# Kernel tuning notes

Hardware: AMD Instinct MI355X
Metric: run time of the kernel (lower is better)

Reference implementation:

```python
import jax, jax.numpy as jnp
import numpy as np

N_NODES = 50000
N_EDGES = 800000
IN_DIM = 5
HID = (32, 64, 128, 64, 32)
OUT_DIM = 2
EPS = 1e-5  # nn.BatchNorm1d default eps


def _bn(x, g, b):
    # BatchNorm1d in training mode: batch (biased) statistics over nodes
    m = jnp.mean(x, axis=0)
    v = jnp.var(x, axis=0)
    return (x - m) * jax.lax.rsqrt(v + EPS) * g + b


def setup_inputs() -> dict:
    key = jax.random.key(0)
    ks = jax.random.split(key, 40)
    it = iter(range(40))
    def nrm(shape, s=0.1):
        return jax.random.normal(ks[next(it)], shape, jnp.float32) * s
    inp = {}
    inp["x"] = jax.random.normal(ks[next(it)], (N_NODES, IN_DIM), jnp.float32)
    inp["edge_index"] = jax.random.randint(ks[next(it)], (2, N_EDGES), 0, N_NODES, jnp.int32)
    # input embedding: Linear(5,32) -> ReLU -> BatchNorm1d(32)
    inp["emb_W"] = nrm((IN_DIM, HID[0]))
    inp["emb_b"] = jnp.zeros((HID[0],), jnp.float32)
    inp["emb_g"] = jnp.ones((HID[0],), jnp.float32)
    inp["emb_beta"] = jnp.zeros((HID[0],), jnp.float32)
    # 4 GraphConv blocks
    for i in range(len(HID) - 1):
        din, dout = HID[i], HID[i + 1]
        inp[f"b{i}_Wrel"] = nrm((din, dout))   # lin_rel weight (has bias)
        inp[f"b{i}_brel"] = jnp.zeros((dout,), jnp.float32)
        inp[f"b{i}_Wroot"] = nrm((din, dout))  # lin_root weight (no bias)
        inp[f"b{i}_g"] = jnp.ones((dout,), jnp.float32)
        inp[f"b{i}_beta"] = jnp.zeros((dout,), jnp.float32)
    # output MLP: Linear(32,16) -> ReLU -> Linear(16,2)
    inp["out_W1"] = nrm((HID[-1], HID[-1] // 2))
    inp["out_b1"] = jnp.zeros((HID[-1] // 2,), jnp.float32)
    inp["out_W2"] = nrm((HID[-1] // 2, OUT_DIM))
    inp["out_b2"] = jnp.zeros((OUT_DIM,), jnp.float32)
    return inp


def reference(x, edge_index,
              emb_W, emb_b, emb_g, emb_beta,
              b0_Wrel, b0_brel, b0_Wroot, b0_g, b0_beta,
              b1_Wrel, b1_brel, b1_Wroot, b1_g, b1_beta,
              b2_Wrel, b2_brel, b2_Wroot, b2_g, b2_beta,
              b3_Wrel, b3_brel, b3_Wroot, b3_g, b3_beta,
              out_W1, out_b1, out_W2, out_b2):
    src, dst = edge_index[0], edge_index[1]
    # input embedding: Linear -> ReLU -> BN
    h = jnp.maximum(x @ emb_W + emb_b, 0.0)
    h = _bn(h, emb_g, emb_beta)
    blocks = [
        (b0_Wrel, b0_brel, b0_Wroot, b0_g, b0_beta),
        (b1_Wrel, b1_brel, b1_Wroot, b1_g, b1_beta),
        (b2_Wrel, b2_brel, b2_Wroot, b2_g, b2_beta),
        (b3_Wrel, b3_brel, b3_Wroot, b3_g, b3_beta),
    ]
    for Wrel, brel, Wroot, g, beta in blocks:
        # GraphConv (aggr='add'): lin_rel(sum_{j in N(i)} x_j) + lin_root(x_i)
        agg = jax.ops.segment_sum(h[src], dst, num_segments=N_NODES)
        h = agg @ Wrel + brel + h @ Wroot
        # BN then ReLU (GNNBlock order)
        h = jnp.maximum(_bn(h, g, beta), 0.0)
    # output MLP
    h = jnp.maximum(h @ out_W1 + out_b1, 0.0)
    return h @ out_W2 + out_b2
```

## Files before the change

kernel.cpp:

```cpp
#include <hip/hip_runtime.h>

#define N_NODES 50000
#define N_EDGES 800000
#define BN_EPS 1e-5f

__device__ __forceinline__ void fma4(float4& a, float s, const float4& w) {
    a.x += s * w.x; a.y += s * w.y; a.z += s * w.z; a.w += s * w.w;
}
__device__ __forceinline__ void add4(float4& a, const float4& b) {
    a.x += b.x; a.y += b.y; a.z += b.z; a.w += b.w;
}

__global__ void zero_i(int* __restrict__ p, int n) {
    int i = blockIdx.x * blockDim.x + threadIdx.x;
    int stride = gridDim.x * blockDim.x;
    for (; i < n; i += stride) p[i] = 0;
}

__global__ void hist_kernel(const int* __restrict__ dst, int* __restrict__ cnt) {
    int i = blockIdx.x * blockDim.x + threadIdx.x;
    int stride = gridDim.x * blockDim.x;
    for (; i < N_EDGES; i += stride) atomicAdd(&cnt[dst[i]], 1);
}
__global__ void scan1_kernel(const int* __restrict__ cnt, int* __restrict__ rp,
                             int* __restrict__ bsum) {
    __shared__ int s[256];
    int t = threadIdx.x;
    int idx = blockIdx.x * 256 + t;
    int v = (idx < N_NODES) ? cnt[idx] : 0;
    s[t] = v;
    __syncthreads();
    for (int off = 1; off < 256; off <<= 1) {
        int x = 0;
        if (t >= off) x = s[t - off];
        __syncthreads();
        s[t] += x;
        __syncthreads();
    }
    if (idx < N_NODES) rp[idx] = s[t] - v;
    if (t == 255) bsum[blockIdx.x] = s[255];
}
__global__ void scan2_kernel(int* __restrict__ bsum, int nb, float* __restrict__ stats) {
    __shared__ int s[256];
    int t = threadIdx.x;
    for (int i = t; i < 5 * 256; i += 256) stats[i] = 0.f;
    int v = (t < nb) ? bsum[t] : 0;
    s[t] = v;
    __syncthreads();
    for (int off = 1; off < 256; off <<= 1) {
        int x = 0;
        if (t >= off) x = s[t - off];
        __syncthreads();
        s[t] += x;
        __syncthreads();
    }
    if (t < nb) bsum[t] = s[t] - v;
}
__global__ void scan3_kernel(int* __restrict__ rp, const int* __restrict__ bsum,
                             int* __restrict__ cnt) {
    int idx = blockIdx.x * 256 + threadIdx.x;
    if (idx < N_NODES) {
        rp[idx] += bsum[blockIdx.x];
        cnt[idx] = 0;
    }
    if (idx == 0) rp[N_NODES] = N_EDGES;
}
__global__ void fill_kernel(const int* __restrict__ src, const int* __restrict__ dst,
                            const int* __restrict__ rp, int* __restrict__ cur,
                            int* __restrict__ ssrc) {
    int i = blockIdx.x * blockDim.x + threadIdx.x;
    int stride = gridDim.x * blockDim.x;
    for (; i < N_EDGES; i += stride) {
        int d = dst[i];
        int p = rp[d] + atomicAdd(&cur[d], 1);
        ssrc[p] = src[i];
    }
}

__global__ __launch_bounds__(256) void emb_fused(
    const float* __restrict__ x, const float* __restrict__ W,
    const float* __restrict__ b, float* __restrict__ out,
    float* __restrict__ stats) {
    __shared__ float lsum[32], lssq[32];
    if (threadIdx.x < 32) { lsum[threadIdx.x] = 0.f; lssq[threadIdx.x] = 0.f; }
    __syncthreads();
    const int o = threadIdx.x & 31;
    const int total = N_NODES * 32;
    float mys = 0.f, myq = 0.f;
    for (int base = blockIdx.x * 256; base < total; base += gridDim.x * 256) {
        int idx = base + threadIdx.x;
        float acc = 0.f;
        if (idx < total) {
            int n = idx >> 5;
            const float* xr = x + n * 5;
            acc = b[o];
#pragma unroll
            for (int k = 0; k < 5; ++k) acc += xr[k] * W[k * 32 + o];
            acc = fmaxf(acc, 0.f);
            out[idx] = acc;
        }
        mys += acc;
        myq += acc * acc;
    }
    mys += __shfl_xor(mys, 32);
    myq += __shfl_xor(myq, 32);
    if ((threadIdx.x & 63) < 32) { atomicAdd(&lsum[o], mys); atomicAdd(&lssq[o], myq); }
    __syncthreads();
    if (threadIdx.x < 32) {
        atomicAdd(&stats[threadIdx.x], lsum[threadIdx.x]);
        atomicAdd(&stats[32 + threadIdx.x], lssq[threadIdx.x]);
    }
}

__global__ __launch_bounds__(256) void bn_apply(
    float4* __restrict__ h, const float* __restrict__ g,
    const float* __restrict__ beta, const float* __restrict__ stats,
    int logD, int relu) {
    const int D = 1 << logD;
    const int total4 = N_NODES << (logD - 2);
    const float invN = 1.f / (float)N_NODES;
    int idx = blockIdx.x * blockDim.x + threadIdx.x;
    int stride = gridDim.x * blockDim.x;
    for (; idx < total4; idx += stride) {
        int f = (idx & ((D >> 2) - 1)) << 2;
        float4 v = h[idx];
        float* vp = (float*)&v;
#pragma unroll
        for (int c = 0; c < 4; ++c) {
            float m = stats[f + c] * invN;
            float var = stats[D + f + c] * invN - m * m;
            float y = (vp[c] - m) * rsqrtf(var + BN_EPS) * g[f + c] + beta[f + c];
            if (relu) y = fmaxf(y, 0.f);
            vp[c] = y;
        }
        h[idx] = v;
    }
}

template <int LOGD>
__global__ __launch_bounds__(256) void gather_agg(
    const float* __restrict__ h, const int* __restrict__ rp,
    const int* __restrict__ ssrc, float4* __restrict__ agg) {
    constexpr int QSH = LOGD - 2;
    int tid = blockIdx.x * 256 + threadIdx.x;
    int node = tid >> QSH;
    if (node >= N_NODES) return;
    int q = tid & ((1 << QSH) - 1);
    int e0 = rp[node], e1 = rp[node + 1];
    float4 acc = make_float4(0.f, 0.f, 0.f, 0.f);
    int e = e0;
    for (; e + 4 <= e1; e += 4) {
        int s0 = ssrc[e], s1 = ssrc[e + 1], s2 = ssrc[e + 2], s3 = ssrc[e + 3];
        float4 v0 = ((const float4*)(h + ((size_t)s0 << LOGD)))[q];
        float4 v1 = ((const float4*)(h + ((size_t)s1 << LOGD)))[q];
        float4 v2 = ((const float4*)(h + ((size_t)s2 << LOGD)))[q];
        float4 v3 = ((const float4*)(h + ((size_t)s3 << LOGD)))[q];
        add4(v0, v1); add4(v2, v3); add4(acc, v0); add4(acc, v2);
    }
    for (; e < e1; ++e) {
        float4 v = ((const float4*)(h + ((size_t)ssrc[e] << LOGD)))[q];
        add4(acc, v);
    }
    agg[tid] = acc;
}

template <int DIN, int DOUT, int OBL>
__global__ __launch_bounds__(256) void gconv_lds(
    const float* __restrict__ h, const float* __restrict__ agg,
    const float* __restrict__ Wrel, const float* __restrict__ brel,
    const float* __restrict__ Wroot, float* __restrict__ out,
    float* __restrict__ stats_out) {
    constexpr int LPN = OBL / 4;
    constexpr int SLOTS = 256 / LPN;
    constexpr int NPT = 4;
    constexpr int KS = 8;
    constexpr int TOT4 = DIN * OBL / 4;
    __shared__ __align__(16) float wl[2 * DIN * OBL];
    __shared__ float lsum[OBL], lssq[OBL];
    const int ob0 = blockIdx.y * OBL;
    for (int e4 = threadIdx.x; e4 < TOT4; e4 += 256) {
        int k = e4 / (OBL / 4);
        int j = (e4 % (OBL / 4)) * 4;
        ((float4*)wl)[e4] = *(const float4*)(Wrel + (size_t)k * DOUT + ob0 + j);
        ((float4*)wl)[TOT4 + e4] = *(const float4*)(Wroot + (size_t)k * DOUT + ob0 + j);
    }
    if (threadIdx.x < OBL) { lsum[threadIdx.x] = 0.f; lssq[threadIdx.x] = 0.f; }
    __syncthreads();

    const int q = threadIdx.x & (LPN - 1);
    const int slot = threadIdx.x / LPN;
    const int o0 = ob0 + q * 4;
    const int nbase = blockIdx.x * (SLOTS * NPT) + slot;

    float4 bias = *(const float4*)(brel + o0);
    float4 acc[NPT];
#pragma unroll
    for (int i = 0; i < NPT; ++i) acc[i] = bias;

#pragma unroll 1
    for (int s = 0; s < DIN / KS; ++s) {
        const int k0 = s * KS;
        float4 hv[NPT][2], av[NPT][2];
#pragma unroll
        for (int i = 0; i < NPT; ++i) {
            int n = nbase + i * SLOTS;
            int nn = (n < N_NODES) ? n : 0;
            const float4* hr = (const float4*)(h + (size_t)nn * DIN + k0);
            const float4* ar = (const float4*)(agg + (size_t)nn * DIN + k0);
            hv[i][0] = hr[0]; hv[i][1] = hr[1];
            av[i][0] = ar[0]; av[i][1] = ar[1];
        }
#pragma unroll
        for (int kk = 0; kk < KS; ++kk) {
            float4 wr = *(const float4*)&wl[(k0 + kk) * OBL + q * 4];
            float4 wo = *(const float4*)&wl[DIN * OBL + (k0 + kk) * OBL + q * 4];
#pragma unroll
            for (int i = 0; i < NPT; ++i) {
                float a  = ((const float*)av[i])[kk];
                float hh = ((const float*)hv[i])[kk];
                fma4(acc[i], a, wr);
                fma4(acc[i], hh, wo);
            }
        }
    }
#pragma unroll
    for (int i = 0; i < NPT; ++i) {
        int n = nbase + i * SLOTS;
        if (n < N_NODES)
            *(float4*)(out + (size_t)n * DOUT + o0) = acc[i];
        else
            acc[i] = make_float4(0.f, 0.f, 0.f, 0.f);
    }
    float4 s4 = make_float4(0.f, 0.f, 0.f, 0.f);
    float4 q4 = make_float4(0.f, 0.f, 0.f, 0.f);
#pragma unroll
    for (int i = 0; i < NPT; ++i) {
        s4.x += acc[i].x; s4.y += acc[i].y; s4.z += acc[i].z; s4.w += acc[i].w;
        q4.x += acc[i].x * acc[i].x; q4.y += acc[i].y * acc[i].y;
        q4.z += acc[i].z * acc[i].z; q4.w += acc[i].w * acc[i].w;
    }
#pragma unroll
    for (int d = LPN; d < 64; d <<= 1) {
        s4.x += __shfl_xor(s4.x, d); s4.y += __shfl_xor(s4.y, d);
        s4.z += __shfl_xor(s4.z, d); s4.w += __shfl_xor(s4.w, d);
        q4.x += __shfl_xor(q4.x, d); q4.y += __shfl_xor(q4.y, d);
        q4.z += __shfl_xor(q4.z, d); q4.w += __shfl_xor(q4.w, d);
    }
    if ((threadIdx.x & 63) < LPN) {
        int c = q * 4;
        atomicAdd(&lsum[c + 0], s4.x); atomicAdd(&lsum[c + 1], s4.y);
        atomicAdd(&lsum[c + 2], s4.z); atomicAdd(&lsum[c + 3], s4.w);
        atomicAdd(&lssq[c + 0], q4.x); atomicAdd(&lssq[c + 1], q4.y);
        atomicAdd(&lssq[c + 2], q4.z); atomicAdd(&lssq[c + 3], q4.w);
    }
    __syncthreads();
    if (threadIdx.x < OBL) {
        atomicAdd(&stats_out[ob0 + threadIdx.x], lsum[threadIdx.x]);
        atomicAdd(&stats_out[DOUT + ob0 + threadIdx.x], lssq[threadIdx.x]);
    }
}

template <int DIN, int DOUT, int OBL>
__global__ __launch_bounds__(256) void prem_lds(
    const float* __restrict__ h, const float* __restrict__ Wrel,
    const float* __restrict__ brel, const float* __restrict__ Wroot,
    float* __restrict__ P, float* __restrict__ Q) {
    constexpr int LPN = OBL / 4;
    constexpr int SLOTS = 256 / LPN;
    constexpr int NPT = 4;
    constexpr int KS = 8;
    constexpr int TOT4 = DIN * OBL / 4;
    __shared__ __align__(16) float wl[2 * DIN * OBL];
    const int ob0 = blockIdx.y * OBL;
    for (int e4 = threadIdx.x; e4 < TOT4; e4 += 256) {
        int k = e4 / (OBL / 4);
        int j = (e4 % (OBL / 4)) * 4;
        ((float4*)wl)[e4] = *(const float4*)(Wrel + (size_t)k * DOUT + ob0 + j);
        ((float4*)wl)[TOT4 + e4] = *(const float4*)(Wroot + (size_t)k * DOUT + ob0 + j);
    }
    __syncthreads();

    const int q = threadIdx.x & (LPN - 1);
    const int slot = threadIdx.x / LPN;
    const int o0 = ob0 + q * 4;
    const int nbase = blockIdx.x * (SLOTS * NPT) + slot;

    float4 bias = *(const float4*)(brel + o0);
    float4 accp[NPT], accq[NPT];
#pragma unroll
    for (int i = 0; i < NPT; ++i) {
        accp[i] = make_float4(0.f, 0.f, 0.f, 0.f);
        accq[i] = bias;
    }

#pragma unroll 1
    for (int s = 0; s < DIN / KS; ++s) {
        const int k0 = s * KS;
        float4 hv[NPT][2];
#pragma unroll
        for (int i = 0; i < NPT; ++i) {
            int n = nbase + i * SLOTS;
            int nn = (n < N_NODES) ? n : 0;
            const float4* hr = (const float4*)(h + (size_t)nn * DIN + k0);
            hv[i][0] = hr[0]; hv[i][1] = hr[1];
        }
#pragma unroll
        for (int kk = 0; kk < KS; ++kk) {
            float4 wr = *(const float4*)&wl[(k0 + kk) * OBL + q * 4];
            float4 wo = *(const float4*)&wl[DIN * OBL + (k0 + kk) * OBL + q * 4];
#pragma unroll
            for (int i = 0; i < NPT; ++i) {
                float hh = ((const float*)hv[i])[kk];
                fma4(accp[i], hh, wr);
                fma4(accq[i], hh, wo);
            }
        }
    }
#pragma unroll
    for (int i = 0; i < NPT; ++i) {
        int n = nbase + i * SLOTS;
        if (n < N_NODES) {
            *(float4*)(P + (size_t)n * DOUT + o0) = accp[i];
            *(float4*)(Q + (size_t)n * DOUT + o0) = accq[i];
        }
    }
}

template <int LOGD>
__global__ __launch_bounds__(256) void gather_add_fused(
    const float* __restrict__ P, const int* __restrict__ rp,
    const int* __restrict__ ssrc, float4* __restrict__ out,
    float* __restrict__ stats) {
    constexpr int D = 1 << LOGD;
    constexpr int Q4 = D / 4;
    __shared__ float lsum[D], lssq[D];
    if (threadIdx.x < D) { lsum[threadIdx.x] = 0.f; lssq[threadIdx.x] = 0.f; }
    __syncthreads();

    const int total = N_NODES * Q4;
    const int q = threadIdx.x & (Q4 - 1);
    float4 mys = make_float4(0.f, 0.f, 0.f, 0.f);
    float4 myq = make_float4(0.f, 0.f, 0.f, 0.f);

    for (int base = blockIdx.x * 256; base < total; base += gridDim.x * 256) {
        int tid = base + threadIdx.x;
        float4 acc = make_float4(0.f, 0.f, 0.f, 0.f);
        if (tid < total) {
            int node = tid >> (LOGD - 2);
            int e0 = rp[node], e1 = rp[node + 1];
            acc = out[tid];
            int e = e0;
            for (; e + 4 <= e1; e += 4) {
                int s0 = ssrc[e], s1 = ssrc[e + 1], s2 = ssrc[e + 2], s3 = ssrc[e + 3];
                float4 v0 = ((const float4*)(P + ((size_t)s0 << LOGD)))[q];
                float4 v1 = ((const float4*)(P + ((size_t)s1 << LOGD)))[q];
                float4 v2 = ((const float4*)(P + ((size_t)s2 << LOGD)))[q];
                float4 v3 = ((const float4*)(P + ((size_t)s3 << LOGD)))[q];
                add4(v0, v1); add4(v2, v3); add4(acc, v0); add4(acc, v2);
            }
            for (; e < e1; ++e) {
                float4 v = ((const float4*)(P + ((size_t)ssrc[e] << LOGD)))[q];
                add4(acc, v);
            }
            out[tid] = acc;
        }
        mys.x += acc.x; mys.y += acc.y; mys.z += acc.z; mys.w += acc.w;
        myq.x += acc.x * acc.x; myq.y += acc.y * acc.y;
        myq.z += acc.z * acc.z; myq.w += acc.w * acc.w;
    }
#pragma unroll
    for (int d = Q4; d < 64; d <<= 1) {
        mys.x += __shfl_xor(mys.x, d); mys.y += __shfl_xor(mys.y, d);
        mys.z += __shfl_xor(mys.z, d); mys.w += __shfl_xor(mys.w, d);
        myq.x += __shfl_xor(myq.x, d); myq.y += __shfl_xor(myq.y, d);
        myq.z += __shfl_xor(myq.z, d); myq.w += __shfl_xor(myq.w, d);
    }
    if ((threadIdx.x & 63) < Q4) {
        atomicAdd(&lsum[4 * q + 0], mys.x); atomicAdd(&lsum[4 * q + 1], mys.y);
        atomicAdd(&lsum[4 * q + 2], mys.z); atomicAdd(&lsum[4 * q + 3], mys.w);
        atomicAdd(&lssq[4 * q + 0], myq.x); atomicAdd(&lssq[4 * q + 1], myq.y);
        atomicAdd(&lssq[4 * q + 2], myq.z); atomicAdd(&lssq[4 * q + 3], myq.w);
    }
    __syncthreads();
    if (threadIdx.x < D) {
        atomicAdd(&stats[threadIdx.x], lsum[threadIdx.x]);
        atomicAdd(&stats[D + threadIdx.x], lssq[threadIdx.x]);
    }
}

__global__ __launch_bounds__(256) void outmlp_kernel(
    const float* __restrict__ h, const float* __restrict__ stats,
    const float* __restrict__ g, const float* __restrict__ beta,
    const float* __restrict__ W1, const float* __restrict__ b1,
    const float* __restrict__ W2, const float* __restrict__ b2,
    float* __restrict__ out) {
    int n = blockIdx.x * 256 + threadIdx.x;
    if (n >= N_NODES) return;
    const float invN = 1.f / (float)N_NODES;
    const float4* hr4 = (const float4*)(h + (size_t)n * 32);
    float hv[32];
#pragma unroll
    for (int k4 = 0; k4 < 8; ++k4) {
        float4 v = hr4[k4];
        float* vp = (float*)&v;
#pragma unroll
        for (int c = 0; c < 4; ++c) {
            int f = 4 * k4 + c;
            float m = stats[f] * invN;
            float var = stats[32 + f] * invN - m * m;
            hv[f] = fmaxf((vp[c] - m) * rsqrtf(var + BN_EPS) * g[f] + beta[f], 0.f);
        }
    }
    float hid[16];
#pragma unroll
    for (int j = 0; j < 16; ++j) hid[j] = b1[j];
#pragma unroll
    for (int k = 0; k < 32; ++k) {
        float hk = hv[k];
#pragma unroll
        for (int j = 0; j < 16; ++j) hid[j] += hk * W1[k * 16 + j];
    }
    float o0 = b2[0], o1 = b2[1];
#pragma unroll
    for (int j = 0; j < 16; ++j) {
        float t = fmaxf(hid[j], 0.f);
        o0 += t * W2[j * 2 + 0];
        o1 += t * W2[j * 2 + 1];
    }
    out[n * 2 + 0] = o0;
    out[n * 2 + 1] = o1;
}

extern "C" void kernel_launch(void* const* d_in, const int* in_sizes, int n_in,
                              void* d_out, int out_size, void* d_ws, size_t ws_size,
                              hipStream_t stream) {
    const float* x        = (const float*)d_in[0];
    const int*   ei       = (const int*)d_in[1];
    const int*   src      = ei;
    const int*   dst      = ei + N_EDGES;
    const float* emb_W    = (const float*)d_in[2];
    const float* emb_b    = (const float*)d_in[3];
    const float* emb_g    = (const float*)d_in[4];
    const float* emb_beta = (const float*)d_in[5];
    const float* out_W1   = (const float*)d_in[26];
    const float* out_b1   = (const float*)d_in[27];
    const float* out_W2   = (const float*)d_in[28];
    const float* out_b2   = (const float*)d_in[29];

    float* ws = (float*)d_ws;
    const size_t HMAX = (size_t)N_NODES * 128;
    float* hA    = ws;
    float* hB    = ws + HMAX;
    float* P     = ws + 2 * HMAX;
    float* stats = ws + 2 * HMAX + (size_t)N_NODES * 64;
    int*   rp    = (int*)(stats + 5 * 256);
    int*   cnt   = rp + N_NODES + 1;
    int*   bsum  = cnt + N_NODES;
    int*   ssrc  = bsum + 256;

    float* st0 = stats;
    float* st1 = stats + 256;
    float* st2 = stats + 512;
    float* st3 = stats + 768;
    float* st4 = stats + 1024;

    const int BS = 256;
    const int NB = (N_NODES + BS - 1) / BS;

    zero_i<<<64, BS, 0, stream>>>(cnt, N_NODES);
    hist_kernel<<<1024, BS, 0, stream>>>(dst, cnt);
    scan1_kernel<<<NB, 256, 0, stream>>>(cnt, rp, bsum);
    scan2_kernel<<<1, 256, 0, stream>>>(bsum, NB, stats);
    scan3_kernel<<<NB, 256, 0, stream>>>(rp, bsum, cnt);
    fill_kernel<<<1024, BS, 0, stream>>>(src, dst, rp, cnt, ssrc);

    emb_fused<<<512, BS, 0, stream>>>(x, emb_W, emb_b, hA, st0);
    bn_apply<<<1563, BS, 0, stream>>>((float4*)hA, emb_g, emb_beta, st0, 5, 0);

    gather_agg<5><<<(N_NODES * 8 + BS - 1) / BS, BS, 0, stream>>>(hA, rp, ssrc, (float4*)P);
    gconv_lds<32, 64, 32><<<dim3((N_NODES + 127) / 128, 2), BS, 0, stream>>>(
        hA, P, (const float*)d_in[6], (const float*)d_in[7], (const float*)d_in[8], hB, st1);
    bn_apply<<<2048, BS, 0, stream>>>((float4*)hB, (const float*)d_in[9], (const float*)d_in[10], st1, 6, 1);

    gather_agg<6><<<(N_NODES * 16 + BS - 1) / BS, BS, 0, stream>>>(hB, rp, ssrc, (float4*)P);
    gconv_lds<64, 128, 32><<<dim3((N_NODES + 127) / 128, 4), BS, 0, stream>>>(
        hB, P, (const float*)d_in[11], (const float*)d_in[12], (const float*)d_in[13], hA, st2);
    bn_apply<<<2048, BS, 0, stream>>>((float4*)hA, (const float*)d_in[14], (const float*)d_in[15], st2, 7, 1);

    prem_lds<128, 64, 16><<<dim3((N_NODES + 255) / 256, 4), BS, 0, stream>>>(
        hA, (const float*)d_in[16], (const float*)d_in[17], (const float*)d_in[18], P, hB);
    gather_add_fused<6><<<512, BS, 0, stream>>>(P, rp, ssrc, (float4*)hB, st3);
    bn_apply<<<2048, BS, 0, stream>>>((float4*)hB, (const float*)d_in[19], (const float*)d_in[20], st3, 6, 1);

    prem_lds<64, 32, 16><<<dim3((N_NODES + 255) / 256, 2), BS, 0, stream>>>(
        hB, (const float*)d_in[21], (const float*)d_in[22], (const float*)d_in[23], P, hA);
    gather_add_fused<5><<<512, BS, 0, stream>>>(P, rp, ssrc, (float4*)hA, st4);

    outmlp_kernel<<<NB, BS, 0, stream>>>(
        hA, st4, (const float*)d_in[24], (const float*)d_in[25],
        out_W1, out_b1, out_W2, out_b2, (float*)d_out);
}
```

Baseline: 392.6 us.

## Fold BatchNorm apply into consuming GraphConv and premultiply kernels

Removes three standalone bn_apply passes: the embedding BN, block-1 BN and block-2 BN. Each consumer kernel now computes BN scale and shift per feature in LDS and applies them to its inputs while loading. For the first GraphConv the aggregated sum of normalized neighbours is rebuilt algebraically as scale*agg + deg*shift, using the in-degree counts. This saves full read/write passes over node features, in exchange for a little extra arithmetic in the matmul inner loops and a BN finalize per block.

```diff
diff --git a/kernel.cpp b/kernel.cpp
--- a/kernel.cpp
+++ b/kernel.cpp
@@ -110,6 +110,21 @@
         atomicAdd(&stats[threadIdx.x], lsum[threadIdx.x]);
         atomicAdd(&stats[32 + threadIdx.x], lssq[threadIdx.x]);
     }
+}
+
+template <int D>
+__device__ __forceinline__ void bn_finalize_lds(
+    const float* __restrict__ stats, const float* __restrict__ g,
+    const float* __restrict__ beta, float* sc, float* sh) {
+    const float invN = 1.f / (float)N_NODES;
+    for (int f = threadIdx.x; f < D; f += 256) {
+        float m = stats[f] * invN;
+        float var = stats[D + f] * invN - m * m;
+        float a = g[f] * rsqrtf(var + BN_EPS);
+        sc[f] = a;
+        sh[f] = beta[f] - m * a;
+    }
+    __syncthreads();
 }
 
 __global__ __launch_bounds__(256) void bn_apply(
@@ -165,6 +180,117 @@
 }
 
 template <int DIN, int DOUT, int OBL>
+__global__ __launch_bounds__(256) void gconv_bn0(
+    const float* __restrict__ h, const float* __restrict__ agg,
+    const float* __restrict__ Wrel, const float* __restrict__ brel,
+    const float* __restrict__ Wroot, float* __restrict__ out,
+    const float* __restrict__ stats_in, const float* __restrict__ g_in,
+    const float* __restrict__ beta_in, const int* __restrict__ deg,
+    float* __restrict__ stats_out) {
+    constexpr int LPN = OBL / 4;
+    constexpr int SLOTS = 256 / LPN;
+    constexpr int NPT = 4;
+    constexpr int KS = 8;
+    constexpr int TOT4 = DIN * OBL / 4;
+    __shared__ __align__(16) float wl[2 * DIN * OBL];
+    __shared__ __align__(16) float sc[DIN];
+    __shared__ __align__(16) float sh[DIN];
+    __shared__ float lsum[OBL], lssq[OBL];
+    const int ob0 = blockIdx.y * OBL;
+    for (int e4 = threadIdx.x; e4 < TOT4; e4 += 256) {
+        int k = e4 / (OBL / 4);
+        int j = (e4 % (OBL / 4)) * 4;
+        ((float4*)wl)[e4] = *(const float4*)(Wrel + (size_t)k * DOUT + ob0 + j);
+        ((float4*)wl)[TOT4 + e4] = *(const float4*)(Wroot + (size_t)k * DOUT + ob0 + j);
+    }
+    if (threadIdx.x < OBL) { lsum[threadIdx.x] = 0.f; lssq[threadIdx.x] = 0.f; }
+    bn_finalize_lds<DIN>(stats_in, g_in, beta_in, sc, sh);
+
+    const int q = threadIdx.x & (LPN - 1);
+    const int slot = threadIdx.x / LPN;
+    const int o0 = ob0 + q * 4;
+    const int nbase = blockIdx.x * (SLOTS * NPT) + slot;
+
+    float degf[NPT];
+#pragma unroll
+    for (int i = 0; i < NPT; ++i) {
+        int n = nbase + i * SLOTS;
+        degf[i] = (n < N_NODES) ? (float)deg[n] : 0.f;
+    }
+
+    float4 bias = *(const float4*)(brel + o0);
+    float4 acc[NPT];
+#pragma unroll
+    for (int i = 0; i < NPT; ++i) acc[i] = bias;
+
+#pragma unroll 1
+    for (int s = 0; s < DIN / KS; ++s) {
+        const int k0 = s * KS;
+        float4 s2[2] = {((const float4*)sc)[k0 / 4], ((const float4*)sc)[k0 / 4 + 1]};
+        float4 t2[2] = {((const float4*)sh)[k0 / 4], ((const float4*)sh)[k0 / 4 + 1]};
+        const float* scp = (const float*)s2;
+        const float* shp = (const float*)t2;
+        float4 hv[NPT][2], av[NPT][2];
+#pragma unroll
+        for (int i = 0; i < NPT; ++i) {
+            int n = nbase + i * SLOTS;
+            int nn = (n < N_NODES) ? n : 0;
+            const float4* hr = (const float4*)(h + (size_t)nn * DIN + k0);
+            const float4* ar = (const float4*)(agg + (size_t)nn * DIN + k0);
+            hv[i][0] = hr[0]; hv[i][1] = hr[1];
+            av[i][0] = ar[0]; av[i][1] = ar[1];
+        }
+#pragma unroll
+        for (int kk = 0; kk < KS; ++kk) {
+            float4 wr = *(const float4*)&wl[(k0 + kk) * OBL + q * 4];
+            float4 wo = *(const float4*)&wl[DIN * OBL + (k0 + kk) * OBL + q * 4];
+#pragma unroll
+            for (int i = 0; i < NPT; ++i) {
+                float a  = fmaf(((const float*)av[i])[kk], scp[kk], degf[i] * shp[kk]);
+                float hh = fmaf(((const float*)hv[i])[kk], scp[kk], shp[kk]);
+                fma4(acc[i], a, wr);
+                fma4(acc[i], hh, wo);
+            }
+        }
+    }
+#pragma unroll
+    for (int i = 0; i < NPT; ++i) {
+        int n = nbase + i * SLOTS;
+        if (n < N_NODES)
+            *(float4*)(out + (size_t)n * DOUT + o0) = acc[i];
+        else
+            acc[i] = make_float4(0.f, 0.f, 0.f, 0.f);
+    }
+    float4 s4 = make_float4(0.f, 0.f, 0.f, 0.f);
+    float4 q4 = make_float4(0.f, 0.f, 0.f, 0.f);
+#pragma unroll
+    for (int i = 0; i < NPT; ++i) {
+        s4.x += acc[i].x; s4.y += acc[i].y; s4.z += acc[i].z; s4.w += acc[i].w;
+        q4.x += acc[i].x * acc[i].x; q4.y += acc[i].y * acc[i].y;
+        q4.z += acc[i].z * acc[i].z; q4.w += acc[i].w * acc[i].w;
+    }
+#pragma unroll
+    for (int d = LPN; d < 64; d <<= 1) {
+        s4.x += __shfl_xor(s4.x, d); s4.y += __shfl_xor(s4.y, d);
+        s4.z += __shfl_xor(s4.z, d); s4.w += __shfl_xor(s4.w, d);
+        q4.x += __shfl_xor(q4.x, d); q4.y += __shfl_xor(q4.y, d);
+        q4.z += __shfl_xor(q4.z, d); q4.w += __shfl_xor(q4.w, d);
+    }
+    if ((threadIdx.x & 63) < LPN) {
+        int c = q * 4;
+        atomicAdd(&lsum[c + 0], s4.x); atomicAdd(&lsum[c + 1], s4.y);
+        atomicAdd(&lsum[c + 2], s4.z); atomicAdd(&lsum[c + 3], s4.w);
+        atomicAdd(&lssq[c + 0], q4.x); atomicAdd(&lssq[c + 1], q4.y);
+        atomicAdd(&lssq[c + 2], q4.z); atomicAdd(&lssq[c + 3], q4.w);
+    }
+    __syncthreads();
+    if (threadIdx.x < OBL) {
+        atomicAdd(&stats_out[ob0 + threadIdx.x], lsum[threadIdx.x]);
+        atomicAdd(&stats_out[DOUT + ob0 + threadIdx.x], lssq[threadIdx.x]);
+    }
+}
+
+template <int DIN, int DOUT, int OBL>
 __global__ __launch_bounds__(256) void gconv_lds(
     const float* __restrict__ h, const float* __restrict__ agg,
     const float* __restrict__ Wrel, const float* __restrict__ brel,
@@ -216,10 +342,8 @@
             float4 wo = *(const float4*)&wl[DIN * OBL + (k0 + kk) * OBL + q * 4];
 #pragma unroll
             for (int i = 0; i < NPT; ++i) {
-                float a  = ((const float*)av[i])[kk];
-                float hh = ((const float*)hv[i])[kk];
-                fma4(acc[i], a, wr);
-                fma4(acc[i], hh, wo);
+                fma4(acc[i], ((const float*)av[i])[kk], wr);
+                fma4(acc[i], ((const float*)hv[i])[kk], wo);
             }
         }
     }
@@ -261,16 +385,20 @@
 }
 
 template <int DIN, int DOUT, int OBL>
-__global__ __launch_bounds__(256) void prem_lds(
+__global__ __launch_bounds__(256) void prem_bn(
     const float* __restrict__ h, const float* __restrict__ Wrel,
     const float* __restrict__ brel, const float* __restrict__ Wroot,
-    float* __restrict__ P, float* __restrict__ Q) {
+    float* __restrict__ P, float* __restrict__ Q,
+    const float* __restrict__ stats_in, const float* __restrict__ g_in,
+    const float* __restrict__ beta_in) {
     constexpr int LPN = OBL / 4;
     constexpr int SLOTS = 256 / LPN;
     constexpr int NPT = 4;
     constexpr int KS = 8;
     constexpr int TOT4 = DIN * OBL / 4;
     __shared__ __align__(16) float wl[2 * DIN * OBL];
+    __shared__ __align__(16) float sc[DIN];
+    __shared__ __align__(16) float sh[DIN];
     const int ob0 = blockIdx.y * OBL;
     for (int e4 = threadIdx.x; e4 < TOT4; e4 += 256) {
         int k = e4 / (OBL / 4);
@@ -278,7 +406,7 @@
         ((float4*)wl)[e4] = *(const float4*)(Wrel + (size_t)k * DOUT + ob0 + j);
         ((float4*)wl)[TOT4 + e4] = *(const float4*)(Wroot + (size_t)k * DOUT + ob0 + j);
     }
-    __syncthreads();
+    bn_finalize_lds<DIN>(stats_in, g_in, beta_in, sc, sh);
 
     const int q = threadIdx.x & (LPN - 1);
     const int slot = threadIdx.x / LPN;
@@ -296,6 +424,10 @@
 #pragma unroll 1
     for (int s = 0; s < DIN / KS; ++s) {
         const int k0 = s * KS;
+        float4 s2[2] = {((const float4*)sc)[k0 / 4], ((const float4*)sc)[k0 / 4 + 1]};
+        float4 t2[2] = {((const float4*)sh)[k0 / 4], ((const float4*)sh)[k0 / 4 + 1]};
+        const float* scp = (const float*)s2;
+        const float* shp = (const float*)t2;
         float4 hv[NPT][2];
 #pragma unroll
         for (int i = 0; i < NPT; ++i) {
@@ -310,7 +442,7 @@
             float4 wo = *(const float4*)&wl[DIN * OBL + (k0 + kk) * OBL + q * 4];
 #pragma unroll
             for (int i = 0; i < NPT; ++i) {
-                float hh = ((const float*)hv[i])[kk];
+                float hh = fmaxf(fmaf(((const float*)hv[i])[kk], scp[kk], shp[kk]), 0.f);
                 fma4(accp[i], hh, wr);
                 fma4(accq[i], hh, wo);
             }
@@ -475,25 +607,25 @@
     fill_kernel<<<1024, BS, 0, stream>>>(src, dst, rp, cnt, ssrc);
 
     emb_fused<<<512, BS, 0, stream>>>(x, emb_W, emb_b, hA, st0);
-    bn_apply<<<1563, BS, 0, stream>>>((float4*)hA, emb_g, emb_beta, st0, 5, 0);
 
     gather_agg<5><<<(N_NODES * 8 + BS - 1) / BS, BS, 0, stream>>>(hA, rp, ssrc, (float4*)P);
-    gconv_lds<32, 64, 32><<<dim3((N_NODES + 127) / 128, 2), BS, 0, stream>>>(
-        hA, P, (const float*)d_in[6], (const float*)d_in[7], (const float*)d_in[8], hB, st1);
+    gconv_bn0<32, 64, 32><<<dim3((N_NODES + 127) / 128, 2), BS, 0, stream>>>(
+        hA, P, (const float*)d_in[6], (const float*)d_in[7], (const float*)d_in[8], hB,
+        st0, emb_g, emb_beta, cnt, st1);
     bn_apply<<<2048, BS, 0, stream>>>((float4*)hB, (const float*)d_in[9], (const float*)d_in[10], st1, 6, 1);
 
     gather_agg<6><<<(N_NODES * 16 + BS - 1) / BS, BS, 0, stream>>>(hB, rp, ssrc, (float4*)P);
     gconv_lds<64, 128, 32><<<dim3((N_NODES + 127) / 128, 4), BS, 0, stream>>>(
         hB, P, (const float*)d_in[11], (const float*)d_in[12], (const float*)d_in[13], hA, st2);
-    bn_apply<<<2048, BS, 0, stream>>>((float4*)hA, (const float*)d_in[14], (const float*)d_in[15], st2, 7, 1);
-
-    prem_lds<128, 64, 16><<<dim3((N_NODES + 255) / 256, 4), BS, 0, stream>>>(
-        hA, (const float*)d_in[16], (const float*)d_in[17], (const float*)d_in[18], P, hB);
+
+    prem_bn<128, 64, 16><<<dim3((N_NODES + 255) / 256, 4), BS, 0, stream>>>(
+        hA, (const float*)d_in[16], (const float*)d_in[17], (const float*)d_in[18], P, hB,
+        st2, (const float*)d_in[14], (const float*)d_in[15]);
     gather_add_fused<6><<<512, BS, 0, stream>>>(P, rp, ssrc, (float4*)hB, st3);
-    bn_apply<<<2048, BS, 0, stream>>>((float4*)hB, (const float*)d_in[19], (const float*)d_in[20], st3, 6, 1);
-
-    prem_lds<64, 32, 16><<<dim3((N_NODES + 255) / 256, 2), BS, 0, stream>>>(
-        hB, (const float*)d_in[21], (const float*)d_in[22], (const float*)d_in[23], P, hA);
+
+    prem_bn<64, 32, 16><<<dim3((N_NODES + 255) / 256, 2), BS, 0, stream>>>(
+        hB, (const float*)d_in[21], (const float*)d_in[22], (const float*)d_in[23], P, hA,
+        st3, (const float*)d_in[19], (const float*)d_in[20]);
     gather_add_fused<5><<<512, BS, 0, stream>>>(P, rp, ssrc, (float4*)hA, st4);
 
     outmlp_kernel<<<NB, BS, 0, stream>>>(
```

Result: faster. 377.6 us (-3.8%).
